# Kernel optimization log

Measured on AMD Instinct MI355X. Metric: run time of the kernel, lower is better.

The kernel has to match this reference:

```python
import jax, jax.numpy as jnp
import numpy as np

EPS_H = 1.0   # smooth Heaviside / delta regularization
MAX_ITER = 10


def _chan_vese_step(phi, I, dt, lam):
    # phi, I: [B, 512, H, W]
    px = jnp.gradient(phi, axis=3)
    py = jnp.gradient(phi, axis=2)
    nrm = jnp.sqrt(px * px + py * py + 1e-8)
    curv = jnp.gradient(px / nrm, axis=3) + jnp.gradient(py / nrm, axis=2)
    # smooth Heaviside and region means (per batch, per channel)
    H = 0.5 * (1.0 + (2.0 / jnp.pi) * jnp.arctan(phi / EPS_H))
    a1 = jnp.sum(H, axis=(2, 3), keepdims=True)
    a2 = jnp.sum(1.0 - H, axis=(2, 3), keepdims=True)
    c1 = jnp.sum(I * H, axis=(2, 3), keepdims=True) / (a1 + 1e-8)
    c2 = jnp.sum(I * (1.0 - H), axis=(2, 3), keepdims=True) / (a2 + 1e-8)
    delta = (EPS_H / jnp.pi) / (phi * phi + EPS_H * EPS_H)
    force = curv - lam * (I - c1) ** 2 + lam * (I - c2) ** 2
    return phi + dt * delta * force


def setup_inputs() -> dict:
    key = jax.random.key(0)
    ks = jax.random.split(key, 6)
    B, C, Hh, Ww = 8, 256, 64, 64
    contour = jax.random.normal(ks[0], (B, C, Hh, Ww), dtype=jnp.float32)
    g = jax.random.normal(ks[1], (B, C, Hh, Ww), dtype=jnp.float32)
    x = jax.random.normal(ks[2], (B, 2 * C, Hh, Ww), dtype=jnp.float32)
    dt = jnp.array([0.1], dtype=jnp.float32)
    lambda_ = jnp.array([1.0], dtype=jnp.float32)
    # 1x1 conv weights (no bias), stored as [out_ch, in_ch]
    g_w = jax.random.normal(ks[3], (512, C), dtype=jnp.float32) / np.sqrt(C)
    x_w = jax.random.normal(ks[4], (512, 2 * C), dtype=jnp.float32) / np.sqrt(2 * C)
    c_w = jax.random.normal(ks[5], (512, C), dtype=jnp.float32) / np.sqrt(C)
    return {"contour": contour, "g": g, "x": x, "dt": dt, "lambda_": lambda_,
            "g_w": g_w, "x_w": x_w, "c_w": c_w}


def reference(contour, g, x, dt, lambda_, g_w, x_w, c_w):
    # z = relu(g_conv(g)) + x_conv(x); 1x1 convs are per-pixel GEMMs
    z = jax.nn.relu(jnp.einsum('bchw,oc->bohw', g, g_w)) \
        + jnp.einsum('bchw,oc->bohw', x, x_w)
    phi0 = jnp.einsum('bchw,oc->bohw', contour, c_w)
    # bicubic resize of phi0 to z's spatial size is identity (same H, W)
    dts = dt[0]
    lam = lambda_[0]
    def step(phi, _):
        return _chan_vese_step(phi, z, dts, lam), None
    phi, _ = jax.lax.scan(step, phi0, None, length=MAX_ITER)
    return jax.nn.sigmoid(phi)
```

## Files before the change

kernel.cpp:

```cpp
#include <hip/hip_runtime.h>
#include <math.h>

#define PIX 4096
#define O_CH 512
#define CV_PITCH 68

#define WOFF_G 0
#define WOFF_X 131072
#define WOFF_C 393216
#define W_ELEMS 524288

typedef __attribute__((ext_vector_type(8))) short s16x8;
typedef __attribute__((ext_vector_type(4))) float f32x4;
typedef __attribute__((ext_vector_type(2))) float f32x2;

__device__ __forceinline__ unsigned cvt_pk_bf16(float a, float b) {
  unsigned r;
  asm("v_cvt_pk_bf16_f32 %0, %1, %2" : "=v"(r) : "v"(a), "v"(b));
  return r;
}

__global__ __launch_bounds__(256) void conv_w(
    const float* __restrict__ gw, const float* __restrict__ xw,
    const float* __restrict__ cw,
    ushort* __restrict__ WH, ushort* __restrict__ WL)
{
  const int r = blockIdx.y;
  const float* src = (r == 0) ? gw : ((r == 1) ? xw : cw);
  const int n4 = (r == 1) ? 65536 : 32768;
  const int doff = (r == 0) ? WOFF_G : ((r == 1) ? WOFF_X : WOFF_C);
  const int i = blockIdx.x * 256 + threadIdx.x;
  if (i >= n4) return;
  float4 v = ((const float4*)src)[i];
  unsigned h01 = cvt_pk_bf16(v.x, v.y);
  unsigned h23 = cvt_pk_bf16(v.z, v.w);
  float l0 = v.x - __uint_as_float(h01 << 16);
  float l1 = v.y - __uint_as_float(h01 & 0xffff0000u);
  float l2 = v.z - __uint_as_float(h23 << 16);
  float l3 = v.w - __uint_as_float(h23 & 0xffff0000u);
  unsigned lo01 = cvt_pk_bf16(l0, l1);
  unsigned lo23 = cvt_pk_bf16(l2, l3);
  ((uint2*)(WH + doff))[i] = make_uint2(h01, h23);
  ((uint2*)(WL + doff))[i] = make_uint2(lo01, lo23);
}

__global__ __launch_bounds__(512, 4) void mfma_gemm_all(
    const float* __restrict__ g, const float* __restrict__ x,
    const float* __restrict__ contour,
    const ushort* __restrict__ WHg, const ushort* __restrict__ WLg,
    float* __restrict__ z, float* __restrict__ phi0)
{
  __shared__ ushort WHs[8192], WLs[8192], AHs[8192], ALs[8192];
  const int t = threadIdx.x;
  const int lane = t & 63, wave = t >> 6;
  const int wm = wave & 1, wn = wave >> 1;
  const int rowA = lane & 15, kg = lane >> 4;
  const int aph = wave & 1;
  const int akg = wave >> 1;
  const int pb = blockIdx.x * 128, ob = blockIdx.y * 128;
  const int bz = blockIdx.z;
  const bool isZ = bz < 8;
  const int b = isZ ? bz : bz - 8;

  const int woff1 = isZ ? WOFF_G : WOFF_C;
  const float* A1 = (isZ ? g : contour) + (size_t)b * 256 * PIX;
  const float* A2 = x + (size_t)(isZ ? b : 0) * 512 * PIX;
  float* out = (isZ ? z : phi0) + (size_t)b * O_CH * PIX;
  const int nsteps = isZ ? 12 : 4;

  f32x4 acc[4][2];
#pragma unroll
  for (int mi = 0; mi < 4; ++mi)
#pragma unroll
    for (int ni = 0; ni < 2; ++ni) acc[mi][ni] = (f32x4){0.f, 0.f, 0.f, 0.f};

  float pf[2][8];

  {
    const float* acp = A1 + pb + aph * 64 + lane;
#pragma unroll
    for (int ch = 0; ch < 2; ++ch)
#pragma unroll
      for (int j = 0; j < 8; ++j)
        pf[ch][j] = acp[(size_t)(ch * 32 + akg * 8 + j) * PIX];
  }

  for (int st = 0; st < nsteps; ++st) {
    const bool s2 = st >= 4;
    const int K = s2 ? 512 : 256;
    const int woff = s2 ? WOFF_X : woff1;
    const int kb = (s2 ? st - 4 : st) * 64;

    {
      const int o_r = t >> 2, hq = t & 3;
      const size_t wbase = (size_t)woff + (size_t)(ob + o_r) * K + kb + hq * 16;
      const ushort* whrow = WHg + wbase;
      const ushort* wlrow = WLg + wbase;
#pragma unroll
      for (int i = 0; i < 2; ++i) {
        int j = 2 * hq + i;
        int idx = o_r * 64 + ((j ^ (o_r & 7)) << 3);
        *(s16x8*)&WHs[idx] = *(const s16x8*)(whrow + i * 8);
        *(s16x8*)&WLs[idx] = *(const s16x8*)(wlrow + i * 8);
      }
    }
    {
      const int rp = aph * 64 + lane;
#pragma unroll
      for (int ch = 0; ch < 2; ++ch) {
        unsigned h[4], l[4];
#pragma unroll
        for (int j2 = 0; j2 < 4; ++j2) {
          float v0 = pf[ch][2 * j2], v1 = pf[ch][2 * j2 + 1];
          h[j2] = cvt_pk_bf16(v0, v1);
          float lo0 = v0 - __uint_as_float(h[j2] << 16);
          float lo1 = v1 - __uint_as_float(h[j2] & 0xffff0000u);
          l[j2] = cvt_pk_bf16(lo0, lo1);
        }
        int grp = ch * 4 + akg;
        int idx = rp * 64 + ((grp ^ (rp & 7)) << 3);
        *(uint4*)&AHs[idx] = make_uint4(h[0], h[1], h[2], h[3]);
        *(uint4*)&ALs[idx] = make_uint4(l[0], l[1], l[2], l[3]);
      }
    }
    __syncthreads();

    if (st + 1 < nsteps) {
      const bool n2 = (st + 1) >= 4;
      const float* Ab = n2 ? A2 : A1;
      const int kbn = (n2 ? st + 1 - 4 : st + 1) * 64;
      const float* acp = Ab + (size_t)kbn * PIX + pb + aph * 64 + lane;
#pragma unroll
      for (int ch = 0; ch < 2; ++ch)
#pragma unroll
        for (int j = 0; j < 8; ++j)
          pf[ch][j] = acp[(size_t)(ch * 32 + akg * 8 + j) * PIX];
    }

#pragma unroll
    for (int ks = 0; ks < 2; ++ks) {
      s16x8 wh[4], wlv[4], ah[2], alv[2];
#pragma unroll
      for (int mi = 0; mi < 4; ++mi) {
        int row = wm * 64 + mi * 16 + rowA;
        int idx = row * 64 + (((ks * 4 + kg) ^ (row & 7)) << 3);
        wh[mi]  = *(const s16x8*)&WHs[idx];
        wlv[mi] = *(const s16x8*)&WLs[idx];
      }
#pragma unroll
      for (int ni = 0; ni < 2; ++ni) {
        int row = wn * 32 + ni * 16 + rowA;
        int idx = row * 64 + (((ks * 4 + kg) ^ (row & 7)) << 3);
        ah[ni]  = *(const s16x8*)&AHs[idx];
        alv[ni] = *(const s16x8*)&ALs[idx];
      }
#pragma unroll
      for (int mi = 0; mi < 4; ++mi)
#pragma unroll
        for (int ni = 0; ni < 2; ++ni) {
          acc[mi][ni] = __builtin_amdgcn_mfma_f32_16x16x32_bf16(wh[mi],  ah[ni],  acc[mi][ni], 0, 0, 0);
          acc[mi][ni] = __builtin_amdgcn_mfma_f32_16x16x32_bf16(wh[mi],  alv[ni], acc[mi][ni], 0, 0, 0);
          acc[mi][ni] = __builtin_amdgcn_mfma_f32_16x16x32_bf16(wlv[mi], ah[ni],  acc[mi][ni], 0, 0, 0);
        }
    }
    if (isZ && st == 3) {
#pragma unroll
      for (int mi = 0; mi < 4; ++mi)
#pragma unroll
        for (int ni = 0; ni < 2; ++ni)
#pragma unroll
          for (int r = 0; r < 4; ++r) acc[mi][ni][r] = fmaxf(acc[mi][ni][r], 0.f);
    }
    __syncthreads();
  }

  const int orow = (lane >> 4) * 4, pcol = lane & 15;
#pragma unroll
  for (int mi = 0; mi < 4; ++mi)
#pragma unroll
    for (int ni = 0; ni < 2; ++ni)
#pragma unroll
      for (int r = 0; r < 4; ++r)
        out[(size_t)(ob + wm * 64 + mi * 16 + orow + r) * PIX +
            pb + wn * 32 + ni * 16 + pcol] = acc[mi][ni][r];
}

__device__ __forceinline__ float fast_atan(float x) {
  float a = __builtin_fabsf(x);
  float inv = __builtin_amdgcn_rcpf(a);
  bool big = a > 1.f;
  float tt = big ? inv : a;
  float t2 = tt * tt;
  float p = fmaf(t2, 0.0208351f, -0.0851330f);
  p = fmaf(t2, p, 0.1801410f);
  p = fmaf(t2, p, -0.3302995f);
  p = fmaf(t2, p, 0.9998660f);
  p = p * tt;
  float r = big ? (1.57079632679f - p) : p;
  return __builtin_copysignf(r, x);
}

__global__ __launch_bounds__(256, 4) void chanvese(
    const float* __restrict__ zb, float* __restrict__ ob,
    const float* __restrict__ dtp, const float* __restrict__ lamp)
{
  __shared__ float phi_l[64 * CV_PITCH];
  __shared__ float ny_l[64 * CV_PITCH];
  __shared__ float red[12];
  const int t = threadIdx.x;
  const int lane = t & 63, wv = t >> 6;
  const int row = t >> 2, s = t & 3;
  const size_t gbase = (size_t)blockIdx.x * PIX + row * 64 + s * 16;
  const float dtv = dtp[0], lam = lamp[0];
  const float INV_PI = 0.31830988618379067f;
  const float dtpi = dtv * INV_PI;
  const float fy = (row == 0 || row == 63) ? 1.f : 0.5f;
  const float exl = (s == 0) ? 2.f : 1.f;
  const float exr = (s == 3) ? 2.f : 1.f;
  const int my = row * CV_PITCH + s * 16;
  const int ub = ((row == 0) ? 0 : row - 1) * CV_PITCH + s * 16;
  const int db = ((row == 63) ? 63 : row + 1) * CV_PITCH + s * 16;
  const f32x2 eps2 = {1e-8f, 1e-8f};

  f32x2 I2[8], ph2[8], nx2[8];
#pragma unroll
  for (int q = 0; q < 4; ++q) {
    f32x4 iv = *(const f32x4*)(zb + gbase + q * 4);
    f32x4 pv = *(const f32x4*)(ob + gbase + q * 4);
    I2[2 * q]     = (f32x2){iv[0], iv[1]};
    I2[2 * q + 1] = (f32x2){iv[2], iv[3]};
    ph2[2 * q]     = (f32x2){pv[0], pv[1]};
    ph2[2 * q + 1] = (f32x2){pv[2], pv[3]};
    *(f32x4*)&phi_l[my + q * 4] = pv;
  }
  float sI = 0.f, s_at = 0.f, s_iat = 0.f;
#pragma unroll
  for (int p = 0; p < 8; ++p) {
    sI += I2[p].x + I2[p].y;
    float a0 = fast_atan(ph2[p].x), a1 = fast_atan(ph2[p].y);
    s_at += a0 + a1;
    s_iat = fmaf(I2[p].x, a0, fmaf(I2[p].y, a1, s_iat));
  }
#pragma unroll
  for (int off = 32; off; off >>= 1) {
    sI += __shfl_xor(sI, off);
    s_at += __shfl_xor(s_at, off);
    s_iat += __shfl_xor(s_iat, off);
  }
  if (lane == 0) { red[wv] = s_at; red[4 + wv] = s_iat; red[8 + wv] = sI; }
  __syncthreads();
  float S_at = red[0] + red[1] + red[2] + red[3];
  float S_iat = red[4] + red[5] + red[6] + red[7];
  const float sumI = red[8] + red[9] + red[10] + red[11];

  for (int it = 0; it < 10; ++it) {
    float a1 = fmaf(INV_PI, S_at, 2048.f);
    float sIH = fmaf(INV_PI, S_iat, 0.5f * sumI);
    float c1 = sIH * __builtin_amdgcn_rcpf(a1 + 1e-8f);
    float c2 = (sumI - sIH) * __builtin_amdgcn_rcpf(4096.f - a1 + 1e-8f);
    float lam12 = lam * (c1 - c2);
    float ms12 = -(c1 + c2);

    float ls = __shfl(ph2[7].y, lane - 1);
    float rs = __shfl(ph2[0].x, lane + 1);
    float lb = (s == 0) ? ph2[0].x : ls;
    float rb = (s == 3) ? ph2[7].y : rs;
#pragma unroll
    for (int q = 0; q < 4; ++q) {
      f32x4 uv = *(const f32x4*)&phi_l[ub + q * 4];
      f32x4 dv = *(const f32x4*)&phi_l[db + q * 4];
      f32x4 nyo;
#pragma unroll
      for (int e = 0; e < 2; ++e) {
        const int p = 2 * q + e;
        f32x2 u2 = (f32x2){uv[2 * e], uv[2 * e + 1]};
        f32x2 d2 = (f32x2){dv[2 * e], dv[2 * e + 1]};
        f32x2 py = (d2 - u2) * fy;
        f32x2 L = {(p == 0) ? lb : ph2[p - 1].y, ph2[p].x};
        f32x2 R = {ph2[p].y, (p == 7) ? rb : ph2[p + 1].x};
        f32x2 px = (R - L) * 0.5f;
        if (p == 0) px.x *= exl;
        if (p == 7) px.y *= exr;
        f32x2 qq = px * px + (py * py + eps2);
        f32x2 rn = {__builtin_amdgcn_rsqf(qq.x), __builtin_amdgcn_rsqf(qq.y)};
        nx2[p] = px * rn;
        f32x2 nyv = py * rn;
        nyo[2 * e] = nyv.x;
        nyo[2 * e + 1] = nyv.y;
      }
      *(f32x4*)&ny_l[my + q * 4] = nyo;
    }
    __syncthreads();

    float nls = __shfl(nx2[7].y, lane - 1);
    float nrs = __shfl(nx2[0].x, lane + 1);
    float nlb = (s == 0) ? nx2[0].x : nls;
    float nrb = (s == 3) ? nx2[7].y : nrs;
    f32x2 inc_at2 = {0.f, 0.f}, inc_iat2 = {0.f, 0.f};
#pragma unroll
    for (int q = 0; q < 4; ++q) {
      f32x4 au = *(const f32x4*)&ny_l[ub + q * 4];
      f32x4 ad = *(const f32x4*)&ny_l[db + q * 4];
      f32x4 pho;
#pragma unroll
      for (int e = 0; e < 2; ++e) {
        const int p = 2 * q + e;
        f32x2 nyu = (f32x2){au[2 * e], au[2 * e + 1]};
        f32x2 nyd = (f32x2){ad[2 * e], ad[2 * e + 1]};
        f32x2 dny = (nyd - nyu) * fy;
        f32x2 L = {(p == 0) ? nlb : nx2[p - 1].y, nx2[p].x};
        f32x2 R = {nx2[p].y, (p == 7) ? nrb : nx2[p + 1].x};
        f32x2 dnx = (R - L) * 0.5f;
        if (p == 0) dnx.x *= exl;
        if (p == 7) dnx.y *= exr;
        f32x2 curv = dnx + dny;
        f32x2 c = ph2[p];
        f32x2 den = c * c + (f32x2){1.f, 1.f};
        f32x2 rcd = {__builtin_amdgcn_rcpf(den.x), __builtin_amdgcn_rcpf(den.y)};
        f32x2 tI = I2[p] * 2.f + (f32x2){ms12, ms12};
        f32x2 force = tI * lam12 + curv;
        f32x2 dphi = (rcd * dtpi) * force;
        f32x2 pn = c + dphi;
        ph2[p] = pn;
        pho[2 * e] = pn.x;
        pho[2 * e + 1] = pn.y;
        f32x2 da = dphi * rcd;
        inc_at2 += da;
        inc_iat2 = I2[p] * da + inc_iat2;
      }
      if (it < 9) *(f32x4*)&phi_l[my + q * 4] = pho;
    }
    if (it < 9) {
      float inc_at = inc_at2.x + inc_at2.y;
      float inc_iat = inc_iat2.x + inc_iat2.y;
#pragma unroll
      for (int off = 32; off; off >>= 1) {
        inc_at += __shfl_xor(inc_at, off);
        inc_iat += __shfl_xor(inc_iat, off);
      }
      if (lane == 0) { red[2 * wv] = inc_at; red[2 * wv + 1] = inc_iat; }
      __syncthreads();
      S_at += red[0] + red[2] + red[4] + red[6];
      S_iat += red[1] + red[3] + red[5] + red[7];
    }
  }

#pragma unroll
  for (int q = 0; q < 4; ++q) {
    f32x2 pa = ph2[2 * q], pb2 = ph2[2 * q + 1];
    float o0 = 1.f / (1.f + exp2f(pa.x * -1.44269504089f));
    float o1 = 1.f / (1.f + exp2f(pa.y * -1.44269504089f));
    float o2 = 1.f / (1.f + exp2f(pb2.x * -1.44269504089f));
    float o3 = 1.f / (1.f + exp2f(pb2.y * -1.44269504089f));
    *(float4*)(ob + gbase + q * 4) = make_float4(o0, o1, o2, o3);
  }
}

extern "C" void kernel_launch(void* const* d_in, const int* in_sizes, int n_in,
                              void* d_out, int out_size, void* d_ws, size_t ws_size,
                              hipStream_t stream)
{
  const float* contour = (const float*)d_in[0];
  const float* g       = (const float*)d_in[1];
  const float* x       = (const float*)d_in[2];
  const float* dt      = (const float*)d_in[3];
  const float* lam     = (const float*)d_in[4];
  const float* g_w     = (const float*)d_in[5];
  const float* x_w     = (const float*)d_in[6];
  const float* c_w     = (const float*)d_in[7];
  float* out = (float*)d_out;
  float* z   = (float*)d_ws;
  ushort* WH = (ushort*)(z + (size_t)8 * O_CH * PIX);
  ushort* WL = WH + W_ELEMS;

  conv_w<<<dim3(256, 3), dim3(256), 0, stream>>>(g_w, x_w, c_w, WH, WL);
  mfma_gemm_all<<<dim3(32, 4, 16), dim3(512), 0, stream>>>(
      g, x, contour, WH, WL, z, out);
  chanvese<<<dim3(4096), dim3(256), 0, stream>>>(z, out, dt, lam);
}
```

Measured before the change: 245.9 us.

## Process two planes per Chan-Vese block and store normalized y-gradient as bf16

Each chanvese block now handles two independent 64x64 planes, interleaving their work so that barriers and reductions are shared and more independent instructions sit between syncs. The grid is halved and launch bounds are lowered to 2 blocks per SM to allow for the doubled register state. The ny intermediate in LDS is packed to bf16, halving its LDS footprint and traffic. In exchange, the higher register pressure may reduce occupancy, and bf16 ny lowers the precision of the curvature term.

New measurement: 268.2 us. 9.1% more time.

```diff
diff --git a/kernel.cpp b/kernel.cpp
--- a/kernel.cpp
+++ b/kernel.cpp
@@ -4,6 +4,7 @@
 #define PIX 4096
 #define O_CH 512
 #define CV_PITCH 68
+#define NY_PITCH 36
 
 #define WOFF_G 0
 #define WOFF_X 131072
@@ -200,17 +201,18 @@
   return __builtin_copysignf(r, x);
 }
 
-__global__ __launch_bounds__(256, 4) void chanvese(
+__global__ __launch_bounds__(256, 2) void chanvese(
     const float* __restrict__ zb, float* __restrict__ ob,
     const float* __restrict__ dtp, const float* __restrict__ lamp)
 {
-  __shared__ float phi_l[64 * CV_PITCH];
-  __shared__ float ny_l[64 * CV_PITCH];
-  __shared__ float red[12];
+  __shared__ float phi_l[2][64 * CV_PITCH];
+  __shared__ unsigned ny_l[2][64 * NY_PITCH];
+  __shared__ float red[24];
   const int t = threadIdx.x;
   const int lane = t & 63, wv = t >> 6;
   const int row = t >> 2, s = t & 3;
-  const size_t gbase = (size_t)blockIdx.x * PIX + row * 64 + s * 16;
+  const size_t gb0 = (size_t)blockIdx.x * PIX + row * 64 + s * 16;
+  const size_t gb1 = gb0 + (size_t)2048 * PIX;
   const float dtv = dtp[0], lam = lamp[0];
   const float INV_PI = 0.31830988618379067f;
   const float dtpi = dtv * INV_PI;
@@ -220,139 +222,193 @@
   const int my = row * CV_PITCH + s * 16;
   const int ub = ((row == 0) ? 0 : row - 1) * CV_PITCH + s * 16;
   const int db = ((row == 63) ? 63 : row + 1) * CV_PITCH + s * 16;
+  const int myn = row * NY_PITCH + s * 8;
+  const int ubn = ((row == 0) ? 0 : row - 1) * NY_PITCH + s * 8;
+  const int dbn = ((row == 63) ? 63 : row + 1) * NY_PITCH + s * 8;
   const f32x2 eps2 = {1e-8f, 1e-8f};
 
-  f32x2 I2[8], ph2[8], nx2[8];
-#pragma unroll
-  for (int q = 0; q < 4; ++q) {
-    f32x4 iv = *(const f32x4*)(zb + gbase + q * 4);
-    f32x4 pv = *(const f32x4*)(ob + gbase + q * 4);
-    I2[2 * q]     = (f32x2){iv[0], iv[1]};
-    I2[2 * q + 1] = (f32x2){iv[2], iv[3]};
-    ph2[2 * q]     = (f32x2){pv[0], pv[1]};
-    ph2[2 * q + 1] = (f32x2){pv[2], pv[3]};
-    *(f32x4*)&phi_l[my + q * 4] = pv;
+  f32x2 I2[2][8], ph2[2][8], nx2[2][8];
+  float S_at[2], S_iat[2], sumI[2];
+  {
+    float sI[2], sa[2], si[2];
+#pragma unroll
+    for (int pl = 0; pl < 2; ++pl) {
+      const size_t gb = pl ? gb1 : gb0;
+      sI[pl] = 0.f; sa[pl] = 0.f; si[pl] = 0.f;
+#pragma unroll
+      for (int q = 0; q < 4; ++q) {
+        f32x4 iv = *(const f32x4*)(zb + gb + q * 4);
+        f32x4 pv = *(const f32x4*)(ob + gb + q * 4);
+        I2[pl][2 * q]     = (f32x2){iv[0], iv[1]};
+        I2[pl][2 * q + 1] = (f32x2){iv[2], iv[3]};
+        ph2[pl][2 * q]     = (f32x2){pv[0], pv[1]};
+        ph2[pl][2 * q + 1] = (f32x2){pv[2], pv[3]};
+        *(f32x4*)&phi_l[pl][my + q * 4] = pv;
+      }
+#pragma unroll
+      for (int p = 0; p < 8; ++p) {
+        sI[pl] += I2[pl][p].x + I2[pl][p].y;
+        float a0 = fast_atan(ph2[pl][p].x), a1 = fast_atan(ph2[pl][p].y);
+        sa[pl] += a0 + a1;
+        si[pl] = fmaf(I2[pl][p].x, a0, fmaf(I2[pl][p].y, a1, si[pl]));
+      }
+    }
+#pragma unroll
+    for (int off = 32; off; off >>= 1)
+#pragma unroll
+      for (int pl = 0; pl < 2; ++pl) {
+        sI[pl] += __shfl_xor(sI[pl], off);
+        sa[pl] += __shfl_xor(sa[pl], off);
+        si[pl] += __shfl_xor(si[pl], off);
+      }
+    if (lane == 0)
+#pragma unroll
+      for (int pl = 0; pl < 2; ++pl) {
+        red[pl * 12 + wv] = sa[pl];
+        red[pl * 12 + 4 + wv] = si[pl];
+        red[pl * 12 + 8 + wv] = sI[pl];
+      }
+    __syncthreads();
+#pragma unroll
+    for (int pl = 0; pl < 2; ++pl) {
+      S_at[pl]  = red[pl*12+0] + red[pl*12+1] + red[pl*12+2] + red[pl*12+3];
+      S_iat[pl] = red[pl*12+4] + red[pl*12+5] + red[pl*12+6] + red[pl*12+7];
+      sumI[pl]  = red[pl*12+8] + red[pl*12+9] + red[pl*12+10] + red[pl*12+11];
+    }
+    __syncthreads();
   }
-  float sI = 0.f, s_at = 0.f, s_iat = 0.f;
-#pragma unroll
-  for (int p = 0; p < 8; ++p) {
-    sI += I2[p].x + I2[p].y;
-    float a0 = fast_atan(ph2[p].x), a1 = fast_atan(ph2[p].y);
-    s_at += a0 + a1;
-    s_iat = fmaf(I2[p].x, a0, fmaf(I2[p].y, a1, s_iat));
+
+  for (int it = 0; it < 10; ++it) {
+    float lam12[2], ms12[2];
+#pragma unroll
+    for (int pl = 0; pl < 2; ++pl) {
+      float a1 = fmaf(INV_PI, S_at[pl], 2048.f);
+      float sIH = fmaf(INV_PI, S_iat[pl], 0.5f * sumI[pl]);
+      float c1 = sIH * __builtin_amdgcn_rcpf(a1 + 1e-8f);
+      float c2 = (sumI[pl] - sIH) * __builtin_amdgcn_rcpf(4096.f - a1 + 1e-8f);
+      lam12[pl] = lam * (c1 - c2);
+      ms12[pl] = -(c1 + c2);
+    }
+
+#pragma unroll
+    for (int pl = 0; pl < 2; ++pl) {
+      float ls = __shfl(ph2[pl][7].y, lane - 1);
+      float rs = __shfl(ph2[pl][0].x, lane + 1);
+      float lb = (s == 0) ? ph2[pl][0].x : ls;
+      float rb = (s == 3) ? ph2[pl][7].y : rs;
+      unsigned nyp[8];
+#pragma unroll
+      for (int q = 0; q < 4; ++q) {
+        f32x4 uv = *(const f32x4*)&phi_l[pl][ub + q * 4];
+        f32x4 dv = *(const f32x4*)&phi_l[pl][db + q * 4];
+#pragma unroll
+        for (int e = 0; e < 2; ++e) {
+          const int p = 2 * q + e;
+          f32x2 u2 = (f32x2){uv[2 * e], uv[2 * e + 1]};
+          f32x2 d2 = (f32x2){dv[2 * e], dv[2 * e + 1]};
+          f32x2 py = (d2 - u2) * fy;
+          f32x2 L = {(p == 0) ? lb : ph2[pl][p - 1].y, ph2[pl][p].x};
+          f32x2 R = {ph2[pl][p].y, (p == 7) ? rb : ph2[pl][p + 1].x};
+          f32x2 px = (R - L) * 0.5f;
+          if (p == 0) px.x *= exl;
+          if (p == 7) px.y *= exr;
+          f32x2 qq = px * px + (py * py + eps2);
+          f32x2 rn = {__builtin_amdgcn_rsqf(qq.x), __builtin_amdgcn_rsqf(qq.y)};
+          nx2[pl][p] = px * rn;
+          f32x2 nyv = py * rn;
+          nyp[p] = cvt_pk_bf16(nyv.x, nyv.y);
+        }
+      }
+      *(uint4*)&ny_l[pl][myn]     = make_uint4(nyp[0], nyp[1], nyp[2], nyp[3]);
+      *(uint4*)&ny_l[pl][myn + 4] = make_uint4(nyp[4], nyp[5], nyp[6], nyp[7]);
+    }
+    __syncthreads();
+
+    float inc_at[2], inc_iat[2];
+#pragma unroll
+    for (int pl = 0; pl < 2; ++pl) {
+      float nls = __shfl(nx2[pl][7].y, lane - 1);
+      float nrs = __shfl(nx2[pl][0].x, lane + 1);
+      float nlb = (s == 0) ? nx2[pl][0].x : nls;
+      float nrb = (s == 3) ? nx2[pl][7].y : nrs;
+      f32x2 ia2 = {0.f, 0.f}, ii2 = {0.f, 0.f};
+#pragma unroll
+      for (int h = 0; h < 2; ++h) {
+        uint4 au = *(const uint4*)&ny_l[pl][ubn + 4 * h];
+        uint4 ad = *(const uint4*)&ny_l[pl][dbn + 4 * h];
+        unsigned ua[4] = {au.x, au.y, au.z, au.w};
+        unsigned ud[4] = {ad.x, ad.y, ad.z, ad.w};
+        f32x2 phs[4];
+#pragma unroll
+        for (int e = 0; e < 4; ++e) {
+          const int p = 4 * h + e;
+          f32x2 nyu = {__uint_as_float(ua[e] << 16), __uint_as_float(ua[e] & 0xffff0000u)};
+          f32x2 nyd = {__uint_as_float(ud[e] << 16), __uint_as_float(ud[e] & 0xffff0000u)};
+          f32x2 dny = (nyd - nyu) * fy;
+          f32x2 L = {(p == 0) ? nlb : nx2[pl][p - 1].y, nx2[pl][p].x};
+          f32x2 R = {nx2[pl][p].y, (p == 7) ? nrb : nx2[pl][p + 1].x};
+          f32x2 dnx = (R - L) * 0.5f;
+          if (p == 0) dnx.x *= exl;
+          if (p == 7) dnx.y *= exr;
+          f32x2 curv = dnx + dny;
+          f32x2 c = ph2[pl][p];
+          f32x2 den = c * c + (f32x2){1.f, 1.f};
+          f32x2 rcd = {__builtin_amdgcn_rcpf(den.x), __builtin_amdgcn_rcpf(den.y)};
+          f32x2 tI = I2[pl][p] * 2.f + (f32x2){ms12[pl], ms12[pl]};
+          f32x2 force = tI * lam12[pl] + curv;
+          f32x2 dphi = (rcd * dtpi) * force;
+          f32x2 pn = c + dphi;
+          ph2[pl][p] = pn;
+          phs[e] = pn;
+          f32x2 da = dphi * rcd;
+          ia2 += da;
+          ii2 = I2[pl][p] * da + ii2;
+        }
+        if (it < 9) {
+          *(f32x4*)&phi_l[pl][my + 8 * h] =
+              (f32x4){phs[0].x, phs[0].y, phs[1].x, phs[1].y};
+          *(f32x4*)&phi_l[pl][my + 8 * h + 4] =
+              (f32x4){phs[2].x, phs[2].y, phs[3].x, phs[3].y};
+        }
+      }
+      inc_at[pl] = ia2.x + ia2.y;
+      inc_iat[pl] = ii2.x + ii2.y;
+    }
+    if (it < 9) {
+#pragma unroll
+      for (int off = 32; off; off >>= 1) {
+        inc_at[0] += __shfl_xor(inc_at[0], off);
+        inc_iat[0] += __shfl_xor(inc_iat[0], off);
+        inc_at[1] += __shfl_xor(inc_at[1], off);
+        inc_iat[1] += __shfl_xor(inc_iat[1], off);
+      }
+      if (lane == 0) {
+        red[wv * 4 + 0] = inc_at[0];
+        red[wv * 4 + 1] = inc_iat[0];
+        red[wv * 4 + 2] = inc_at[1];
+        red[wv * 4 + 3] = inc_iat[1];
+      }
+      __syncthreads();
+#pragma unroll
+      for (int pl = 0; pl < 2; ++pl) {
+        S_at[pl]  += red[pl*2+0] + red[pl*2+4] + red[pl*2+8] + red[pl*2+12];
+        S_iat[pl] += red[pl*2+1] + red[pl*2+5] + red[pl*2+9] + red[pl*2+13];
+      }
+    }
   }
-#pragma unroll
-  for (int off = 32; off; off >>= 1) {
-    sI += __shfl_xor(sI, off);
-    s_at += __shfl_xor(s_at, off);
-    s_iat += __shfl_xor(s_iat, off);
-  }
-  if (lane == 0) { red[wv] = s_at; red[4 + wv] = s_iat; red[8 + wv] = sI; }
-  __syncthreads();
-  float S_at = red[0] + red[1] + red[2] + red[3];
-  float S_iat = red[4] + red[5] + red[6] + red[7];
-  const float sumI = red[8] + red[9] + red[10] + red[11];
-
-  for (int it = 0; it < 10; ++it) {
-    float a1 = fmaf(INV_PI, S_at, 2048.f);
-    float sIH = fmaf(INV_PI, S_iat, 0.5f * sumI);
-    float c1 = sIH * __builtin_amdgcn_rcpf(a1 + 1e-8f);
-    float c2 = (sumI - sIH) * __builtin_amdgcn_rcpf(4096.f - a1 + 1e-8f);
-    float lam12 = lam * (c1 - c2);
-    float ms12 = -(c1 + c2);
-
-    float ls = __shfl(ph2[7].y, lane - 1);
-    float rs = __shfl(ph2[0].x, lane + 1);
-    float lb = (s == 0) ? ph2[0].x : ls;
-    float rb = (s == 3) ? ph2[7].y : rs;
+
+#pragma unroll
+  for (int pl = 0; pl < 2; ++pl) {
+    const size_t gb = pl ? gb1 : gb0;
 #pragma unroll
     for (int q = 0; q < 4; ++q) {
-      f32x4 uv = *(const f32x4*)&phi_l[ub + q * 4];
-      f32x4 dv = *(const f32x4*)&phi_l[db + q * 4];
-      f32x4 nyo;
-#pragma unroll
-      for (int e = 0; e < 2; ++e) {
-        const int p = 2 * q + e;
-        f32x2 u2 = (f32x2){uv[2 * e], uv[2 * e + 1]};
-        f32x2 d2 = (f32x2){dv[2 * e], dv[2 * e + 1]};
-        f32x2 py = (d2 - u2) * fy;
-        f32x2 L = {(p == 0) ? lb : ph2[p - 1].y, ph2[p].x};
-        f32x2 R = {ph2[p].y, (p == 7) ? rb : ph2[p + 1].x};
-        f32x2 px = (R - L) * 0.5f;
-        if (p == 0) px.x *= exl;
-        if (p == 7) px.y *= exr;
-        f32x2 qq = px * px + (py * py + eps2);
-        f32x2 rn = {__builtin_amdgcn_rsqf(qq.x), __builtin_amdgcn_rsqf(qq.y)};
-        nx2[p] = px * rn;
-        f32x2 nyv = py * rn;
-        nyo[2 * e] = nyv.x;
-        nyo[2 * e + 1] = nyv.y;
-      }
-      *(f32x4*)&ny_l[my + q * 4] = nyo;
-    }
-    __syncthreads();
-
-    float nls = __shfl(nx2[7].y, lane - 1);
-    float nrs = __shfl(nx2[0].x, lane + 1);
-    float nlb = (s == 0) ? nx2[0].x : nls;
-    float nrb = (s == 3) ? nx2[7].y : nrs;
-    f32x2 inc_at2 = {0.f, 0.f}, inc_iat2 = {0.f, 0.f};
-#pragma unroll
-    for (int q = 0; q < 4; ++q) {
-      f32x4 au = *(const f32x4*)&ny_l[ub + q * 4];
-      f32x4 ad = *(const f32x4*)&ny_l[db + q * 4];
-      f32x4 pho;
-#pragma unroll
-      for (int e = 0; e < 2; ++e) {
-        const int p = 2 * q + e;
-        f32x2 nyu = (f32x2){au[2 * e], au[2 * e + 1]};
-        f32x2 nyd = (f32x2){ad[2 * e], ad[2 * e + 1]};
-        f32x2 dny = (nyd - nyu) * fy;
-        f32x2 L = {(p == 0) ? nlb : nx2[p - 1].y, nx2[p].x};
-        f32x2 R = {nx2[p].y, (p == 7) ? nrb : nx2[p + 1].x};
-        f32x2 dnx = (R - L) * 0.5f;
-        if (p == 0) dnx.x *= exl;
-        if (p == 7) dnx.y *= exr;
-        f32x2 curv = dnx + dny;
-        f32x2 c = ph2[p];
-        f32x2 den = c * c + (f32x2){1.f, 1.f};
-        f32x2 rcd = {__builtin_amdgcn_rcpf(den.x), __builtin_amdgcn_rcpf(den.y)};
-        f32x2 tI = I2[p] * 2.f + (f32x2){ms12, ms12};
-        f32x2 force = tI * lam12 + curv;
-        f32x2 dphi = (rcd * dtpi) * force;
-        f32x2 pn = c + dphi;
-        ph2[p] = pn;
-        pho[2 * e] = pn.x;
-        pho[2 * e + 1] = pn.y;
-        f32x2 da = dphi * rcd;
-        inc_at2 += da;
-        inc_iat2 = I2[p] * da + inc_iat2;
-      }
-      if (it < 9) *(f32x4*)&phi_l[my + q * 4] = pho;
-    }
-    if (it < 9) {
-      float inc_at = inc_at2.x + inc_at2.y;
-      float inc_iat = inc_iat2.x + inc_iat2.y;
-#pragma unroll
-      for (int off = 32; off; off >>= 1) {
-        inc_at += __shfl_xor(inc_at, off);
-        inc_iat += __shfl_xor(inc_iat, off);
-      }
-      if (lane == 0) { red[2 * wv] = inc_at; red[2 * wv + 1] = inc_iat; }
-      __syncthreads();
-      S_at += red[0] + red[2] + red[4] + red[6];
-      S_iat += red[1] + red[3] + red[5] + red[7];
-    }
-  }
-
-#pragma unroll
-  for (int q = 0; q < 4; ++q) {
-    f32x2 pa = ph2[2 * q], pb2 = ph2[2 * q + 1];
-    float o0 = 1.f / (1.f + exp2f(pa.x * -1.44269504089f));
-    float o1 = 1.f / (1.f + exp2f(pa.y * -1.44269504089f));
-    float o2 = 1.f / (1.f + exp2f(pb2.x * -1.44269504089f));
-    float o3 = 1.f / (1.f + exp2f(pb2.y * -1.44269504089f));
-    *(float4*)(ob + gbase + q * 4) = make_float4(o0, o1, o2, o3);
+      f32x2 pa = ph2[pl][2 * q], pb2 = ph2[pl][2 * q + 1];
+      float o0 = 1.f / (1.f + exp2f(pa.x * -1.44269504089f));
+      float o1 = 1.f / (1.f + exp2f(pa.y * -1.44269504089f));
+      float o2 = 1.f / (1.f + exp2f(pb2.x * -1.44269504089f));
+      float o3 = 1.f / (1.f + exp2f(pb2.y * -1.44269504089f));
+      *(float4*)(ob + gb + q * 4) = make_float4(o0, o1, o2, o3);
+    }
   }
 }
 
@@ -376,5 +432,5 @@
   conv_w<<<dim3(256, 3), dim3(256), 0, stream>>>(g_w, x_w, c_w, WH, WL);
   mfma_gemm_all<<<dim3(32, 4, 16), dim3(512), 0, stream>>>(
       g, x, contour, WH, WL, z, out);
-  chanvese<<<dim3(4096), dim3(256), 0, stream>>>(z, out, dt, lam);
-}
+  chanvese<<<dim3(2048), dim3(256), 0, stream>>>(z, out, dt, lam);
+}
```
